# Kernel tuning notes

Measured on AMD Instinct MI355X. Metric: run time of the kernel, lower is better.

Reference implementation:

```python
import jax, jax.numpy as jnp
import numpy as np
from jax.scipy.linalg import solve_triangular

S = 64            # number of weight samples (Xi.shape[0])
OUT = 256         # out_channels
IN_CH, K = 64, 3
F = IN_CH * K * K # in_features == inducing_batch == 576
LOG_PREC_INIT = -4.0
LOG_PREC_LR = 1.0


def setup_inputs() -> dict:
    key = jax.random.key(0)
    k1, k2, k3, k4 = jax.random.split(key, 4)
    Xi = jax.random.normal(k1, (S, 128, F), jnp.float32)          # only shape[0] is used
    Xi_param = jax.random.normal(k2, (1, F, F), jnp.float32)      # self.Xi: [1, inducing_batch, in_features]
    u = jax.random.normal(k3, (OUT, F, 1), jnp.float32)           # self.u
    log_prec_scaled = (LOG_PREC_INIT / LOG_PREC_LR) * jnp.ones((1, 1, F), jnp.float32)
    Z = jax.random.normal(k4, (S, OUT, F, 1), jnp.float32)        # internal randn noise, made explicit
    return dict(Xi=Xi, Xi_param=Xi_param, u=u, log_prec_scaled=log_prec_scaled, Z=Z)


def reference(Xi, Xi_param, u, log_prec_scaled, Z):
    S_ = Xi.shape[0]
    Fd = Xi_param.shape[-1]
    O = u.shape[0]
    # log_prec = log_prec_lr * log_prec_scaled  (precs == 1)
    log_prec = LOG_PREC_LR * log_prec_scaled[0]                    # [1, F]
    Xe = jnp.broadcast_to(Xi_param, (S_, Fd, Fd))                  # [S, I, F]
    XiLT = jnp.exp(log_prec) * jnp.swapaxes(Xe, -1, -2)            # [S, F, I]  (prec_L is None branch)
    XiLXi = XiLT @ Xe                                              # [S, F, F]
    XiLY = jnp.einsum('sfi,oi->sfo', XiLT, u[..., 0])              # [S, F, O]  (torch: [S, O, F, 1])
    # NealPrior over in_shape: precision = fan_in * I, fan_in = in_features
    prior_prec = float(Fd)
    prec = XiLXi + prior_prec * jnp.eye(Fd, dtype=XiLXi.dtype)     # [S, F, F]
    L = jnp.linalg.cholesky(prec)
    logdet_prec = 2.0 * jnp.sum(jnp.log(jnp.diagonal(L, axis1=-2, axis2=-1)), -1)  # [S]
    logdet_prec_tot = O * logdet_prec                              # expand(S, O).sum(-1)
    # cholesky_solve(XiLY, L): prec^{-1} XiLY, batched over O via RHS columns
    mean = solve_triangular(L, solve_triangular(L, XiLY, lower=True), lower=True, trans=1)  # [S, F, O]
    Zm = jnp.swapaxes(Z[..., 0], -1, -2)                           # [S, F, O]
    dW = solve_triangular(L, Zm, lower=True, trans=1)              # L^T dW = Z
    sample_fo = mean + dW                                          # [S, F, O]
    sample = jnp.swapaxes(sample_fo, -1, -2)                       # [S, O, F] == self._sample
    # logP = mvnormal_log_prob_unnorm(prior_prec, sample^T):  -0.5 tr(x^T P x) + 0.5*O*logdet(P)
    logP = (-0.5 * prior_prec * jnp.sum(sample_fo ** 2, (-1, -2))
            + 0.5 * O * Fd * jnp.log(jnp.asarray(prior_prec, sample.dtype)))
    logQ = -0.5 * jnp.sum(Z ** 2, (-1, -2, -3)) + 0.5 * logdet_prec_tot
    logpq = logP - logQ                                            # [S]
    return sample, logpq
```

## Files before the change

### kernel.cpp

```cpp
#include <hip/hip_runtime.h>

#define F 576
#define OUTC 256
#define SNUM 64
#define PP 576.0f
#define NBLK 36

__device__ __forceinline__ void gbar(int* cnt, int barid) {
  __syncthreads();
  if (threadIdx.x == 0) {
    __builtin_amdgcn_fence(__ATOMIC_RELEASE, "agent");
    __hip_atomic_fetch_add(cnt, 1, __ATOMIC_RELAXED, __HIP_MEMORY_SCOPE_AGENT);
    int target = barid * NBLK;
    while (__hip_atomic_load(cnt, __ATOMIC_RELAXED, __HIP_MEMORY_SCOPE_AGENT) < target) {
      __builtin_amdgcn_s_sleep(2);
    }
    __builtin_amdgcn_fence(__ATOMIC_ACQUIRE, "agent");
  }
  __syncthreads();
}

__device__ __forceinline__ void mm16(const float (*As)[68], const float (*Bs)[68],
                                     float acc[4][4], int tx, int ty) {
#pragma unroll
  for (int k = 0; k < 32; ++k) {
    float4 a4 = *(const float4*)&As[k][ty * 4];
    float4 b4 = *(const float4*)&Bs[k][tx * 4];
    float av[4] = {a4.x, a4.y, a4.z, a4.w};
    float bv[4] = {b4.x, b4.y, b4.z, b4.w};
#pragma unroll
    for (int r = 0; r < 4; ++r)
#pragma unroll
      for (int c = 0; c < 4; ++c) acc[r][c] += av[r] * bv[c];
  }
}

__device__ void tile_gemm(const float* __restrict__ A, int lda,
                          const float* __restrict__ B, int ldb,
                          float* __restrict__ C, int ldc,
                          int m0, int n0, int K, float sgn,
                          float (*As)[68], float (*Bs)[68]) {
  int t = threadIdx.x, tx = t & 15, ty = t >> 4;
  float acc[4][4] = {};
  for (int k0 = 0; k0 < K; k0 += 32) {
    int rr = t >> 2, kq = t & 3;
    const float* ap = &A[(m0 + rr) * lda + k0 + kq * 8];
    float4 a0 = *(const float4*)ap;
    float4 a1 = *(const float4*)(ap + 4);
    As[kq*8+0][rr] = a0.x; As[kq*8+1][rr] = a0.y;
    As[kq*8+2][rr] = a0.z; As[kq*8+3][rr] = a0.w;
    As[kq*8+4][rr] = a1.x; As[kq*8+5][rr] = a1.y;
    As[kq*8+6][rr] = a1.z; As[kq*8+7][rr] = a1.w;
    int col = t & 63, kr = t >> 6;
#pragma unroll
    for (int kk = 0; kk < 32; kk += 4)
      Bs[kr + kk][col] = B[(k0 + kr + kk) * ldb + n0 + col];
    __syncthreads();
    mm16(As, Bs, acc, tx, ty);
    __syncthreads();
  }
#pragma unroll
  for (int r = 0; r < 4; ++r)
#pragma unroll
    for (int c = 0; c < 4; ++c)
      C[(m0 + ty*4 + r) * ldc + n0 + tx*4 + c] = sgn * acc[r][c];
}

__device__ void diag_factor(float* Ts ) {
  int t = threadIdx.x;
  __syncthreads();
  if (t < 64) {
    int l = t;
    float r[64];
#pragma unroll
    for (int g = 0; g < 64; ++g) r[g] = Ts[l*66 + g];
#pragma unroll
    for (int j = 0; j < 64; ++j) {
      float d = __shfl(r[j], j, 64);
      float inv = 1.0f / sqrtf(d);
      float c = r[j] * inv;
      r[j] = c;
#pragma unroll
      for (int g = j + 1; g < 64; ++g)
        r[g] = fmaf(-__shfl(c, g, 64), c, r[g]);
    }
#pragma unroll
    for (int g = 0; g < 64; ++g) Ts[l*66 + g] = r[g];
  }
  __syncthreads();
}

__device__ void panel_phase(float* __restrict__ G, int k0, int b,
                            float* Ts, float* invd) {
  int t = threadIdx.x;
  for (int idx = t; idx < 64 * 64; idx += 256) {
    int i = idx >> 6, j = idx & 63;
    Ts[i*66 + j] = G[(k0 + i) * F + k0 + j];
  }
  __syncthreads();
  if (t < 64) invd[t] = 1.0f / Ts[t*66 + t];
  __syncthreads();
  int l = t & 63, w = t >> 6;
  int r0 = k0 + 64 + b * 16 + w * 4;
  float v0 = G[(r0 + 0) * F + k0 + l];
  float v1 = G[(r0 + 1) * F + k0 + l];
  float v2 = G[(r0 + 2) * F + k0 + l];
  float v3 = G[(r0 + 3) * F + k0 + l];
#pragma unroll
  for (int j = 0; j < 64; ++j) {
    float dj = invd[j];
    float x0 = __shfl(v0, j, 64) * dj;
    float x1 = __shfl(v1, j, 64) * dj;
    float x2 = __shfl(v2, j, 64) * dj;
    float x3 = __shfl(v3, j, 64) * dj;
    if (l > j) {
      float lj = Ts[l*66 + j];
      v0 = fmaf(-x0, lj, v0);
      v1 = fmaf(-x1, lj, v1);
      v2 = fmaf(-x2, lj, v2);
      v3 = fmaf(-x3, lj, v3);
    }
  }
  float dl = invd[l];
  G[(r0 + 0) * F + k0 + l] = v0 * dl;
  G[(r0 + 1) * F + k0 + l] = v1 * dl;
  G[(r0 + 2) * F + k0 + l] = v2 * dl;
  G[(r0 + 3) * F + k0 + l] = v3 * dl;
}

__device__ void upd_phase(float* __restrict__ G, int k0, int ti, int tj, bool fuse,
                          float (*As)[68], float (*Bs)[68], float* Ts) {
  int b0 = k0 + 64;
  int i0 = b0 + ti * 64, j0 = b0 + tj * 64;
  int t = threadIdx.x, tx = t & 15, ty = t >> 4;
  float acc[4][4] = {};
  for (int kk0 = 0; kk0 < 64; kk0 += 32) {
    for (int idx = t; idx < 64 * 32; idx += 256) {
      int ii = idx >> 5, kk = idx & 31;
      As[kk][ii] = G[(i0 + ii) * F + k0 + kk0 + kk];
      Bs[kk][ii] = G[(j0 + ii) * F + k0 + kk0 + kk];
    }
    __syncthreads();
#pragma unroll
    for (int k = 0; k < 32; ++k) {
      float a[4], b[4];
#pragma unroll
      for (int m = 0; m < 4; ++m) { a[m] = As[k][ty*4 + m]; b[m] = Bs[k][tx*4 + m]; }
#pragma unroll
      for (int r = 0; r < 4; ++r)
#pragma unroll
        for (int c = 0; c < 4; ++c) acc[r][c] += a[r] * b[c];
    }
    __syncthreads();
  }
  if (!fuse) {
#pragma unroll
    for (int r = 0; r < 4; ++r)
#pragma unroll
      for (int c = 0; c < 4; ++c)
        G[(i0 + ty*4 + r) * F + j0 + tx*4 + c] -= acc[r][c];
  } else {
#pragma unroll
    for (int r = 0; r < 4; ++r)
#pragma unroll
      for (int c = 0; c < 4; ++c)
        Ts[(ty*4 + r)*66 + tx*4 + c] =
            G[(i0 + ty*4 + r) * F + j0 + tx*4 + c] - acc[r][c];
    diag_factor(Ts);
    for (int idx = t; idx < 64 * 64; idx += 256) {
      int i = idx >> 6, j = idx & 63;
      if (j <= i) G[(i0 + i) * F + j0 + j] = Ts[i*66 + j];
    }
  }
}

__device__ void base_inv_phase(const float* __restrict__ G, float* __restrict__ LI,
                               int blk, float* Ts, float* invd) {
  int base = blk * 64, t = threadIdx.x;
  for (int idx = t; idx < 64 * 64; idx += 256) {
    int i = idx >> 6, j = idx & 63;
    Ts[i*66 + j] = G[(base + i) * F + base + j];
  }
  __syncthreads();
  if (t < 64) invd[t] = 1.0f / Ts[t*66 + t];
  __syncthreads();
  int l = t & 63, w = t >> 6;
  float v[16];
#pragma unroll
  for (int c = 0; c < 16; ++c) v[c] = (l == (w * 16 + c)) ? 1.0f : 0.0f;
#pragma unroll
  for (int j = 0; j < 64; ++j) {
    float dj = invd[j];
    float lj = (l > j) ? Ts[l*66 + j] : 0.0f;
#pragma unroll
    for (int c = 0; c < 16; ++c) {
      float x = __shfl(v[c], j, 64) * dj;
      v[c] = fmaf(-x, lj, v[c]);
    }
  }
  float dl = invd[l];
#pragma unroll
  for (int c = 0; c < 16; ++c)
    LI[(base + l) * F + base + w * 16 + c] = v[c] * dl;
}

__device__ void mean_phase(const float* __restrict__ LI, const float* __restrict__ T,
                           float* __restrict__ meanT, int bf, int bo,
                           float (*As)[68], float (*Bs)[68]) {
  int t = threadIdx.x, tx = t & 15, ty = t >> 4;
  int f0 = bf * 64, o0 = bo * 64;
  float acc[4][4] = {};
  for (int g0 = f0; g0 < F; g0 += 32) {
    int col = t & 63, kr = t >> 6;
#pragma unroll
    for (int kk = 0; kk < 32; kk += 4) {
      As[kr + kk][col] = T[(g0 + kr + kk) * OUTC + o0 + col];
      Bs[kr + kk][col] = LI[(g0 + kr + kk) * F + f0 + col];
    }
    __syncthreads();
    mm16(As, Bs, acc, tx, ty);
    __syncthreads();
  }
#pragma unroll
  for (int r = 0; r < 4; ++r) {
    float4 st = make_float4(acc[r][0], acc[r][1], acc[r][2], acc[r][3]);
    *(float4*)&meanT[(o0 + ty*4 + r) * F + f0 + tx*4] = st;
  }
}

__global__ __launch_bounds__(256) void k_mid(float* __restrict__ G, float* __restrict__ LI,
                                             const float* __restrict__ Yb,
                                             float* __restrict__ Tb, float* __restrict__ meanT,
                                             int* __restrict__ ctl) {
  __shared__ float As[32][68];
  __shared__ float Bs[32][68];
  __shared__ float Ts[64 * 66];
  __shared__ float invd[64];
  int* cnt = ctl;
  int bar = 0;
  int b = blockIdx.x, t = threadIdx.x;
  float* Tw = Tb;

  if (b == 0) {
    for (int idx = t; idx < 64 * 64; idx += 256) {
      int i = idx >> 6, j = idx & 63;
      Ts[i*66 + j] = G[i * F + j];
    }
    diag_factor(Ts);
    for (int idx = t; idx < 64 * 64; idx += 256) {
      int i = idx >> 6, j = idx & 63;
      if (j <= i) G[i * F + j] = Ts[i*66 + j];
    }
  }
  gbar(cnt, ++bar);

  for (int k = 0; k < 8; ++k) {
    int k0 = k * 64;
    int n = 512 - k0;
    if (b < n / 16) panel_phase(G, k0, b, Ts, invd);
    gbar(cnt, ++bar);
    int nt = n / 64, ntiles = nt * (nt + 1) / 2;
    if (b < ntiles) {
      int ti = 0, bb = b;
      while (bb >= ti + 1) { bb -= ti + 1; ++ti; }
      int tj = bb;
      upd_phase(G, k0, ti, tj, (ti == 0 && tj == 0), As, Bs, Ts);
    }
    gbar(cnt, ++bar);
  }

  if (b < 9) {
    base_inv_phase(G, LI, b, Ts, invd);
  } else {
    int m = b - 9;
    for (int q = m; q < 72; q += 27) {
      int r = q / 8, cc = q % 8;
      int c = cc + (cc >= r ? 1 : 0);
      for (int idx = t; idx < 64 * 16; idx += 256) {
        int i = idx >> 4, jj = idx & 15;
        ((float4*)&LI[(r * 64 + i) * F + c * 64])[jj] = make_float4(0.f, 0.f, 0.f, 0.f);
      }
    }
  }
  gbar(cnt, ++bar);

  if (b < 4) tile_gemm(G + 64*F + b*128*(F+1), F, LI + b*128*(F+1), F,
                       Tw + b*4096, 64, 0, 0, 64, 1.0f, As, Bs);
  gbar(cnt, ++bar);
  if (b < 4) tile_gemm(LI + 64*(F+1) + b*128*(F+1), F, Tw + b*4096, 64,
                       LI + 64*F + b*128*(F+1), F, 0, 0, 64, -1.0f, As, Bs);
  gbar(cnt, ++bar);
  if (b < 8) {
    int z = b >> 2, tl = b & 3;
    tile_gemm(G + 128*F + z*256*(F+1), F, LI + z*256*(F+1), F,
              Tw + z*16384, 128, (tl>>1)*64, (tl&1)*64, 128, 1.0f, As, Bs);
  }
  gbar(cnt, ++bar);
  if (b < 8) {
    int z = b >> 2, tl = b & 3;
    tile_gemm(LI + 128*(F+1) + z*256*(F+1), F, Tw + z*16384, 128,
              LI + 128*F + z*256*(F+1), F, (tl>>1)*64, (tl&1)*64, 128, -1.0f, As, Bs);
  }
  gbar(cnt, ++bar);
  if (b < 16) tile_gemm(G + 256*F, F, LI, F, Tw, 256,
                        (b>>2)*64, (b&3)*64, 256, 1.0f, As, Bs);
  gbar(cnt, ++bar);
  if (b < 16) tile_gemm(LI + 256*(F+1), F, Tw, 256, LI + 256*F, F,
                        (b>>2)*64, (b&3)*64, 256, -1.0f, As, Bs);
  gbar(cnt, ++bar);
  if (b < 8) tile_gemm(G + 512*F, F, LI, F, Tw, 512, 0, b*64, 512, 1.0f, As, Bs);
  gbar(cnt, ++bar);
  if (b < 8) tile_gemm(LI + 512*(F+1), F, Tw, 512, LI + 512*F, F, 0, b*64, 64, -1.0f, As, Bs);
  gbar(cnt, ++bar);

  {
    int bg = b >> 2, bo = b & 3;
    tile_gemm(LI, F, Yb, OUTC, Tb, OUTC, bg * 64, bo * 64, bg * 64 + 64, 1.0f, As, Bs);
  }
  gbar(cnt, ++bar);

  {
    int bf = b >> 2, bo = b & 3;
    mean_phase(LI, Tb, meanT, bf, bo, As, Bs);
  }
}

__global__ __launch_bounds__(256) void k_gy(const float* __restrict__ X,
                                            const float* __restrict__ u,
                                            const float* __restrict__ lp,
                                            float* __restrict__ G,
                                            float* __restrict__ Y) {
  __shared__ float As[32][68];
  __shared__ float Bs[32][68];
  int t = threadIdx.x, tx = t & 15, ty = t >> 4;
  if (blockIdx.z == 0) {
    int bi = blockIdx.y, bj = blockIdx.x;
    if (bj > bi) return;
    int f0 = bi * 64, g0 = bj * 64;
    float acc[4][4] = {};
    for (int i0 = 0; i0 < F; i0 += 32) {
      int col = t & 63, kr = t >> 6;
#pragma unroll
      for (int kk = 0; kk < 32; kk += 4) {
        int i = i0 + kr + kk;
        float e = expf(lp[i]);
        As[kr + kk][col] = e * X[i * F + f0 + col];
        Bs[kr + kk][col] = X[i * F + g0 + col];
      }
      __syncthreads();
      mm16(As, Bs, acc, tx, ty);
      __syncthreads();
    }
#pragma unroll
    for (int r = 0; r < 4; ++r) {
      int gr = f0 + ty*4 + r;
#pragma unroll
      for (int c = 0; c < 4; ++c) {
        int gc = g0 + tx*4 + c;
        float v = acc[r][c];
        if (gr == gc) v += PP;
        G[gr * F + gc] = v;
      }
    }
  } else {
    if (blockIdx.x >= 4) return;
    int bo = blockIdx.x, bf = blockIdx.y;
    int f0 = bf * 64, o0 = bo * 64;
    float acc[4][4] = {};
    for (int i0 = 0; i0 < F; i0 += 32) {
      {
        int col = t & 63, kr = t >> 6;
#pragma unroll
        for (int kk = 0; kk < 32; kk += 4) {
          int i = i0 + kr + kk;
          As[kr + kk][col] = expf(lp[i]) * X[i * F + f0 + col];
        }
        int oo = t >> 2, kq = t & 3;
        const float* ur = &u[(o0 + oo) * F + i0 + kq * 8];
        float4 u0 = *(const float4*)ur;
        float4 u1 = *(const float4*)(ur + 4);
        Bs[kq*8+0][oo] = u0.x; Bs[kq*8+1][oo] = u0.y;
        Bs[kq*8+2][oo] = u0.z; Bs[kq*8+3][oo] = u0.w;
        Bs[kq*8+4][oo] = u1.x; Bs[kq*8+5][oo] = u1.y;
        Bs[kq*8+6][oo] = u1.z; Bs[kq*8+7][oo] = u1.w;
      }
      __syncthreads();
      mm16(As, Bs, acc, tx, ty);
      __syncthreads();
    }
#pragma unroll
    for (int r = 0; r < 4; ++r) {
      float4 st = make_float4(acc[r][0], acc[r][1], acc[r][2], acc[r][3]);
      *(float4*)&Y[(f0 + ty*4 + r) * OUTC + o0 + tx*4] = st;
    }
  }
}

__global__ __launch_bounds__(256) void k_big(const float* __restrict__ Z,
                                             const float* __restrict__ LI,
                                             const float* __restrict__ meanT,
                                             float* __restrict__ out,
                                             double* __restrict__ parts) {
  int bf = blockIdx.x, br = blockIdx.y;
  __shared__ float As[32][68];
  __shared__ float Bs[32][68];
  __shared__ double redA[256];
  __shared__ double redB[256];
  int t = threadIdx.x, tx = t & 15, ty = t >> 4;
  int f0 = bf * 64, r0 = br * 64;
  float acc[4][4] = {};
  double zsq = 0.0;
  for (int g0 = f0; g0 < F; g0 += 32) {
    {
      int rr = t >> 2, kq = t & 3;
      const float* zr = &Z[(r0 + rr) * F + g0 + kq * 8];
      float4 a0 = *(const float4*)zr;
      float4 a1 = *(const float4*)(zr + 4);
      if (bf == 0) {
        zsq += (double)a0.x*a0.x + (double)a0.y*a0.y + (double)a0.z*a0.z + (double)a0.w*a0.w
             + (double)a1.x*a1.x + (double)a1.y*a1.y + (double)a1.z*a1.z + (double)a1.w*a1.w;
      }
      As[kq*8+0][rr] = a0.x; As[kq*8+1][rr] = a0.y;
      As[kq*8+2][rr] = a0.z; As[kq*8+3][rr] = a0.w;
      As[kq*8+4][rr] = a1.x; As[kq*8+5][rr] = a1.y;
      As[kq*8+6][rr] = a1.z; As[kq*8+7][rr] = a1.w;
      int col = t & 63, kr = t >> 6;
#pragma unroll
      for (int kk = 0; kk < 32; kk += 4)
        Bs[kr + kk][col] = LI[(g0 + kr + kk) * F + f0 + col];
    }
    __syncthreads();
    mm16(As, Bs, acc, tx, ty);
    __syncthreads();
  }
  double ssq = 0.0;
#pragma unroll
  for (int r = 0; r < 4; ++r) {
    int row = r0 + ty*4 + r;
    int o = row & 255;
    float4 mv = *(const float4*)&meanT[o * F + f0 + tx*4];
    float4 st = make_float4(acc[r][0] + mv.x, acc[r][1] + mv.y,
                            acc[r][2] + mv.z, acc[r][3] + mv.w);
    *(float4*)&out[row * F + f0 + tx*4] = st;
    ssq += (double)st.x*st.x + (double)st.y*st.y + (double)st.z*st.z + (double)st.w*st.w;
  }
  redA[t] = ssq; redB[t] = zsq;
  __syncthreads();
  for (int o = 128; o > 0; o >>= 1) {
    if (t < o) { redA[t] += redA[t + o]; redB[t] += redB[t + o]; }
    __syncthreads();
  }
  if (t == 0) {
    int s = br >> 2;
    atomicAdd(&parts[s * 2 + 0], redA[0]);
    if (bf == 0) atomicAdd(&parts[s * 2 + 1], redB[0]);
  }
}

__global__ __launch_bounds__(576) void k_logpq_final(const float* __restrict__ LI,
                                                     const double* __restrict__ parts,
                                                     float* __restrict__ out) {
  __shared__ double red[576];
  int t = threadIdx.x;
  red[t] = log((double)LI[t * F + t]);
  __syncthreads();
  for (int o = 512; o > 0; o >>= 1) {
    if (t < o && t + o < 576) red[t] += red[t + o];
    __syncthreads();
  }
  double ldsumLI = red[0];
  if (t < SNUM) {
    double ssq = parts[t * 2 + 0];
    double zsq = parts[t * 2 + 1];
    double pp = 576.0;
    double lpq = -0.5 * pp * ssq
               + 0.5 * (double)(OUTC * F) * log(pp)
               + 0.5 * zsq
               + (double)OUTC * ldsumLI;
    out[SNUM * OUTC * F + t] = (float)lpq;
  }
}

extern "C" void kernel_launch(void* const* d_in, const int* in_sizes, int n_in,
                              void* d_out, int out_size, void* d_ws, size_t ws_size,
                              hipStream_t stream) {
  (void)in_sizes; (void)n_in; (void)out_size; (void)ws_size;
  const float* X  = (const float*)d_in[1];
  const float* u  = (const float*)d_in[2];
  const float* lp = (const float*)d_in[3];
  const float* Z  = (const float*)d_in[4];
  float* out = (float*)d_out;

  float* ws    = (float*)d_ws;
  float* G     = ws;
  float* LI    = ws + 331776;
  float* Yb    = ws + 663552;
  float* Tb    = ws + 811008;
  float* meanT = ws + 958464;
  double* parts = (double*)(ws + 1105920);
  int*    ctl   = (int*)(ws + 1105920 + 256);

  hipMemsetAsync((void*)(ws + 1105920), 0, 1032, stream);
  k_gy<<<dim3(9, 9, 2), 256, 0, stream>>>(X, u, lp, G, Yb);
  k_mid<<<NBLK, 256, 0, stream>>>(G, LI, Yb, Tb, meanT, ctl);
  k_big<<<dim3(9, 256), 256, 0, stream>>>(Z, LI, meanT, out, parts);
  k_logpq_final<<<1, 576, 0, stream>>>(LI, parts, out);
}
```

Before: 699.6 us.

## Use flag-based master grid barrier and merge dependent GEMM phases

```diff
diff --git a/kernel.cpp b/kernel.cpp
--- a/kernel.cpp
+++ b/kernel.cpp
@@ -5,15 +5,24 @@
 #define SNUM 64
 #define PP 576.0f
 #define NBLK 36
-
-__device__ __forceinline__ void gbar(int* cnt, int barid) {
+#define FLAG_STRIDE 32
+
+__device__ __forceinline__ void gbar(int* flags, int* gen, int b, int barid) {
   __syncthreads();
   if (threadIdx.x == 0) {
     __builtin_amdgcn_fence(__ATOMIC_RELEASE, "agent");
-    __hip_atomic_fetch_add(cnt, 1, __ATOMIC_RELAXED, __HIP_MEMORY_SCOPE_AGENT);
-    int target = barid * NBLK;
-    while (__hip_atomic_load(cnt, __ATOMIC_RELAXED, __HIP_MEMORY_SCOPE_AGENT) < target) {
-      __builtin_amdgcn_s_sleep(2);
+    __hip_atomic_store(&flags[b * FLAG_STRIDE], barid, __ATOMIC_RELAXED, __HIP_MEMORY_SCOPE_AGENT);
+    if (b == 0) {
+      for (int i = 1; i < NBLK; ++i) {
+        while (__hip_atomic_load(&flags[i * FLAG_STRIDE], __ATOMIC_RELAXED, __HIP_MEMORY_SCOPE_AGENT) < barid) {
+          __builtin_amdgcn_s_sleep(1);
+        }
+      }
+      __hip_atomic_store(gen, barid, __ATOMIC_RELAXED, __HIP_MEMORY_SCOPE_AGENT);
+    } else {
+      while (__hip_atomic_load(gen, __ATOMIC_RELAXED, __HIP_MEMORY_SCOPE_AGENT) < barid) {
+        __builtin_amdgcn_s_sleep(1);
+      }
     }
     __builtin_amdgcn_fence(__ATOMIC_ACQUIRE, "agent");
   }
@@ -231,12 +240,11 @@
 __global__ __launch_bounds__(256) void k_mid(float* __restrict__ G, float* __restrict__ LI,
                                              const float* __restrict__ Yb,
                                              float* __restrict__ Tb, float* __restrict__ meanT,
-                                             int* __restrict__ ctl) {
+                                             int* __restrict__ gen, int* __restrict__ flags) {
   __shared__ float As[32][68];
   __shared__ float Bs[32][68];
   __shared__ float Ts[64 * 66];
   __shared__ float invd[64];
-  int* cnt = ctl;
   int bar = 0;
   int b = blockIdx.x, t = threadIdx.x;
   float* Tw = Tb;
@@ -252,13 +260,13 @@
       if (j <= i) G[i * F + j] = Ts[i*66 + j];
     }
   }
-  gbar(cnt, ++bar);
+  gbar(flags, gen, b, ++bar);
 
   for (int k = 0; k < 8; ++k) {
     int k0 = k * 64;
     int n = 512 - k0;
     if (b < n / 16) panel_phase(G, k0, b, Ts, invd);
-    gbar(cnt, ++bar);
+    gbar(flags, gen, b, ++bar);
     int nt = n / 64, ntiles = nt * (nt + 1) / 2;
     if (b < ntiles) {
       int ti = 0, bb = b;
@@ -266,7 +274,7 @@
       int tj = bb;
       upd_phase(G, k0, ti, tj, (ti == 0 && tj == 0), As, Bs, Ts);
     }
-    gbar(cnt, ++bar);
+    gbar(flags, gen, b, ++bar);
   }
 
   if (b < 9) {
@@ -282,42 +290,44 @@
       }
     }
   }
-  gbar(cnt, ++bar);
-
-  if (b < 4) tile_gemm(G + 64*F + b*128*(F+1), F, LI + b*128*(F+1), F,
-                       Tw + b*4096, 64, 0, 0, 64, 1.0f, As, Bs);
-  gbar(cnt, ++bar);
-  if (b < 4) tile_gemm(LI + 64*(F+1) + b*128*(F+1), F, Tw + b*4096, 64,
-                       LI + 64*F + b*128*(F+1), F, 0, 0, 64, -1.0f, As, Bs);
-  gbar(cnt, ++bar);
+  gbar(flags, gen, b, ++bar);
+
+  if (b < 4) {
+    tile_gemm(G + 64*F + b*128*(F+1), F, LI + b*128*(F+1), F,
+              Tw + b*4096, 64, 0, 0, 64, 1.0f, As, Bs);
+    tile_gemm(LI + 64*(F+1) + b*128*(F+1), F, Tw + b*4096, 64,
+              LI + 64*F + b*128*(F+1), F, 0, 0, 64, -1.0f, As, Bs);
+  }
+  gbar(flags, gen, b, ++bar);
   if (b < 8) {
     int z = b >> 2, tl = b & 3;
     tile_gemm(G + 128*F + z*256*(F+1), F, LI + z*256*(F+1), F,
               Tw + z*16384, 128, (tl>>1)*64, (tl&1)*64, 128, 1.0f, As, Bs);
   }
-  gbar(cnt, ++bar);
+  gbar(flags, gen, b, ++bar);
   if (b < 8) {
     int z = b >> 2, tl = b & 3;
     tile_gemm(LI + 128*(F+1) + z*256*(F+1), F, Tw + z*16384, 128,
               LI + 128*F + z*256*(F+1), F, (tl>>1)*64, (tl&1)*64, 128, -1.0f, As, Bs);
   }
-  gbar(cnt, ++bar);
+  gbar(flags, gen, b, ++bar);
   if (b < 16) tile_gemm(G + 256*F, F, LI, F, Tw, 256,
                         (b>>2)*64, (b&3)*64, 256, 1.0f, As, Bs);
-  gbar(cnt, ++bar);
+  gbar(flags, gen, b, ++bar);
   if (b < 16) tile_gemm(LI + 256*(F+1), F, Tw, 256, LI + 256*F, F,
                         (b>>2)*64, (b&3)*64, 256, -1.0f, As, Bs);
-  gbar(cnt, ++bar);
-  if (b < 8) tile_gemm(G + 512*F, F, LI, F, Tw, 512, 0, b*64, 512, 1.0f, As, Bs);
-  gbar(cnt, ++bar);
-  if (b < 8) tile_gemm(LI + 512*(F+1), F, Tw, 512, LI + 512*F, F, 0, b*64, 64, -1.0f, As, Bs);
-  gbar(cnt, ++bar);
+  gbar(flags, gen, b, ++bar);
+  if (b < 8) {
+    tile_gemm(G + 512*F, F, LI, F, Tw, 512, 0, b*64, 512, 1.0f, As, Bs);
+    tile_gemm(LI + 512*(F+1), F, Tw, 512, LI + 512*F, F, 0, b*64, 64, -1.0f, As, Bs);
+  }
+  gbar(flags, gen, b, ++bar);
 
   {
     int bg = b >> 2, bo = b & 3;
     tile_gemm(LI, F, Yb, OUTC, Tb, OUTC, bg * 64, bo * 64, bg * 64 + 64, 1.0f, As, Bs);
   }
-  gbar(cnt, ++bar);
+  gbar(flags, gen, b, ++bar);
 
   {
     int bf = b >> 2, bo = b & 3;
@@ -498,11 +508,12 @@
   float* Tb    = ws + 811008;
   float* meanT = ws + 958464;
   double* parts = (double*)(ws + 1105920);
-  int*    ctl   = (int*)(ws + 1105920 + 256);
-
-  hipMemsetAsync((void*)(ws + 1105920), 0, 1032, stream);
+  int*    gen   = (int*)(ws + 1105920 + 256);
+  int*    flags = (int*)(ws + 1105920 + 288);
+
+  hipMemsetAsync((void*)(ws + 1105920), 0, 8192, stream);
   k_gy<<<dim3(9, 9, 2), 256, 0, stream>>>(X, u, lp, G, Yb);
-  k_mid<<<NBLK, 256, 0, stream>>>(G, LI, Yb, Tb, meanT, ctl);
+  k_mid<<<NBLK, 256, 0, stream>>>(G, LI, Yb, Tb, meanT, gen, flags);
   k_big<<<dim3(9, 256), 256, 0, stream>>>(Z, LI, meanT, out, parts);
   k_logpq_final<<<1, 576, 0, stream>>>(LI, parts, out);
 }
```

Measured after the change: 942.2 us. +34.7%, slower.

## Replace recursive blocked L-inverse with column-strip forward/backward substitution solves

Applied to the files above, without the earlier changes.

```diff
diff --git a/kernel.cpp b/kernel.cpp
--- a/kernel.cpp
+++ b/kernel.cpp
@@ -35,35 +35,148 @@
   }
 }
 
-__device__ void tile_gemm(const float* __restrict__ A, int lda,
-                          const float* __restrict__ B, int ldb,
-                          float* __restrict__ C, int ldc,
-                          int m0, int n0, int K, float sgn,
-                          float (*As)[68], float (*Bs)[68]) {
+__device__ __forceinline__ void mmqs(const float (*As)[68], const float (*Xs)[20],
+                                     float acc[4], int tx, int ty) {
+#pragma unroll
+  for (int k = 0; k < 32; ++k) {
+    float4 a4 = *(const float4*)&As[k][ty * 4];
+    float b = Xs[k][tx];
+    acc[0] += a4.x * b; acc[1] += a4.y * b;
+    acc[2] += a4.z * b; acc[3] += a4.w * b;
+  }
+}
+
+__device__ __forceinline__ void stageA_T(const float* __restrict__ M, int lda, int h,
+                                         float (*As)[68]) {
+  int t = threadIdx.x, rr = t >> 2, kq = t & 3;
+  const float* ap = &M[rr * lda + h * 32 + kq * 8];
+  float4 a0 = *(const float4*)ap;
+  float4 a1 = *(const float4*)(ap + 4);
+  As[kq*8+0][rr] = a0.x; As[kq*8+1][rr] = a0.y;
+  As[kq*8+2][rr] = a0.z; As[kq*8+3][rr] = a0.w;
+  As[kq*8+4][rr] = a1.x; As[kq*8+5][rr] = a1.y;
+  As[kq*8+6][rr] = a1.z; As[kq*8+7][rr] = a1.w;
+}
+
+__device__ __forceinline__ void stageA_N(const float* __restrict__ M, int lda, int h,
+                                         float (*As)[68]) {
+  int t = threadIdx.x, col = t & 63, kr = t >> 6;
+#pragma unroll
+  for (int kk = 0; kk < 32; kk += 4)
+    As[kr + kk][col] = M[(h * 32 + kr + kk) * lda + col];
+}
+
+__device__ __forceinline__ void stageX(const float* __restrict__ src, int ldx, int c0, int h,
+                                       float (*Xs)[20]) {
+  int t = threadIdx.x, k = t >> 3, c = (t & 7) * 2;
+  Xs[k][c]     = src[(h * 32 + k) * ldx + c0 + c];
+  Xs[k][c + 1] = src[(h * 32 + k) * ldx + c0 + c + 1];
+}
+
+__device__ __forceinline__ void stageX_T(const float* __restrict__ src, int ldsrc, int c0,
+                                         int poff, int h, float (*Xs)[20]) {
+  int t = threadIdx.x, k = t >> 3, c = (t & 7) * 2;
+  Xs[k][c]     = src[(c0 + c) * ldsrc + poff + h * 32 + k];
+  Xs[k][c + 1] = src[(c0 + c + 1) * ldsrc + poff + h * 32 + k];
+}
+
+__device__ void solve_LI(const float* __restrict__ G, float* __restrict__ LI,
+                         int j, int q, float (*As)[68], float (*Xs)[20]) {
   int t = threadIdx.x, tx = t & 15, ty = t >> 4;
-  float acc[4][4] = {};
-  for (int k0 = 0; k0 < K; k0 += 32) {
-    int rr = t >> 2, kq = t & 3;
-    const float* ap = &A[(m0 + rr) * lda + k0 + kq * 8];
-    float4 a0 = *(const float4*)ap;
-    float4 a1 = *(const float4*)(ap + 4);
-    As[kq*8+0][rr] = a0.x; As[kq*8+1][rr] = a0.y;
-    As[kq*8+2][rr] = a0.z; As[kq*8+3][rr] = a0.w;
-    As[kq*8+4][rr] = a1.x; As[kq*8+5][rr] = a1.y;
-    As[kq*8+6][rr] = a1.z; As[kq*8+7][rr] = a1.w;
-    int col = t & 63, kr = t >> 6;
-#pragma unroll
-    for (int kk = 0; kk < 32; kk += 4)
-      Bs[kr + kk][col] = B[(k0 + kr + kk) * ldb + n0 + col];
-    __syncthreads();
-    mm16(As, Bs, acc, tx, ty);
-    __syncthreads();
-  }
-#pragma unroll
-  for (int r = 0; r < 4; ++r)
-#pragma unroll
-    for (int c = 0; c < 4; ++c)
-      C[(m0 + ty*4 + r) * ldc + n0 + tx*4 + c] = sgn * acc[r][c];
+  int c0 = j * 64 + q * 16;
+  for (int i = j + 1; i <= 8; ++i) {
+    float acc[4] = {0.f, 0.f, 0.f, 0.f};
+    for (int p = j; p < i; ++p)
+      for (int h = 0; h < 2; ++h) {
+        __syncthreads();
+        stageA_T(&G[(i * 64) * F + p * 64], F, h, As);
+        stageX(&LI[(p * 64) * F], F, c0, h, Xs);
+        __syncthreads();
+        mmqs(As, Xs, acc, tx, ty);
+      }
+    float out[4] = {0.f, 0.f, 0.f, 0.f};
+    for (int h = 0; h < 2; ++h) {
+      __syncthreads();
+      if ((ty >> 3) == h) {
+        int rl = (ty & 7) * 4;
+        Xs[rl+0][tx] = -acc[0]; Xs[rl+1][tx] = -acc[1];
+        Xs[rl+2][tx] = -acc[2]; Xs[rl+3][tx] = -acc[3];
+      }
+      stageA_T(&LI[(i * 64) * F + i * 64], F, h, As);
+      __syncthreads();
+      mmqs(As, Xs, out, tx, ty);
+    }
+#pragma unroll
+    for (int m = 0; m < 4; ++m)
+      LI[(i * 64 + ty * 4 + m) * F + c0 + tx] = out[m];
+  }
+}
+
+__device__ void solve_T(const float* __restrict__ G, const float* __restrict__ LI,
+                        const float* __restrict__ Yb, float* __restrict__ Tb,
+                        int q16, float (*As)[68], float (*Xs)[20]) {
+  int t = threadIdx.x, tx = t & 15, ty = t >> 4;
+  int c0 = q16 * 16;
+  for (int i = 0; i <= 8; ++i) {
+    float acc[4] = {0.f, 0.f, 0.f, 0.f};
+    for (int p = 0; p < i; ++p)
+      for (int h = 0; h < 2; ++h) {
+        __syncthreads();
+        stageA_T(&G[(i * 64) * F + p * 64], F, h, As);
+        stageX(&Tb[(p * 64) * OUTC], OUTC, c0, h, Xs);
+        __syncthreads();
+        mmqs(As, Xs, acc, tx, ty);
+      }
+    float out[4] = {0.f, 0.f, 0.f, 0.f};
+    for (int h = 0; h < 2; ++h) {
+      __syncthreads();
+      if ((ty >> 3) == h) {
+        int rl = (ty & 7) * 4;
+#pragma unroll
+        for (int m = 0; m < 4; ++m)
+          Xs[rl + m][tx] = Yb[(i * 64 + h * 32 + rl + m) * OUTC + c0 + tx] - acc[m];
+      }
+      stageA_T(&LI[(i * 64) * F + i * 64], F, h, As);
+      __syncthreads();
+      mmqs(As, Xs, out, tx, ty);
+    }
+#pragma unroll
+    for (int m = 0; m < 4; ++m)
+      Tb[(i * 64 + ty * 4 + m) * OUTC + c0 + tx] = out[m];
+  }
+}
+
+__device__ void solve_M(const float* __restrict__ G, const float* __restrict__ LI,
+                        const float* __restrict__ Tb, float* __restrict__ meanT,
+                        int q16, float (*As)[68], float (*Xs)[20]) {
+  int t = threadIdx.x, tx = t & 15, ty = t >> 4;
+  int c0 = q16 * 16;
+  for (int i = 8; i >= 0; --i) {
+    float acc[4] = {0.f, 0.f, 0.f, 0.f};
+    for (int p = i + 1; p <= 8; ++p)
+      for (int h = 0; h < 2; ++h) {
+        __syncthreads();
+        stageA_N(&G[(p * 64) * F + i * 64], F, h, As);
+        stageX_T(meanT, F, c0, p * 64, h, Xs);
+        __syncthreads();
+        mmqs(As, Xs, acc, tx, ty);
+      }
+    float out[4] = {0.f, 0.f, 0.f, 0.f};
+    for (int h = 0; h < 2; ++h) {
+      __syncthreads();
+      if ((ty >> 3) == h) {
+        int rl = (ty & 7) * 4;
+#pragma unroll
+        for (int m = 0; m < 4; ++m)
+          Xs[rl + m][tx] = Tb[(i * 64 + h * 32 + rl + m) * OUTC + c0 + tx] - acc[m];
+      }
+      stageA_N(&LI[(i * 64) * F + i * 64], F, h, As);
+      __syncthreads();
+      mmqs(As, Xs, out, tx, ty);
+    }
+    float4 st = make_float4(out[0], out[1], out[2], out[3]);
+    *(float4*)&meanT[(c0 + tx) * F + i * 64 + ty * 4] = st;
+  }
 }
 
 __device__ void diag_factor(float* Ts ) {
@@ -204,42 +317,17 @@
     LI[(base + l) * F + base + w * 16 + c] = v[c] * dl;
 }
 
-__device__ void mean_phase(const float* __restrict__ LI, const float* __restrict__ T,
-                           float* __restrict__ meanT, int bf, int bo,
-                           float (*As)[68], float (*Bs)[68]) {
-  int t = threadIdx.x, tx = t & 15, ty = t >> 4;
-  int f0 = bf * 64, o0 = bo * 64;
-  float acc[4][4] = {};
-  for (int g0 = f0; g0 < F; g0 += 32) {
-    int col = t & 63, kr = t >> 6;
-#pragma unroll
-    for (int kk = 0; kk < 32; kk += 4) {
-      As[kr + kk][col] = T[(g0 + kr + kk) * OUTC + o0 + col];
-      Bs[kr + kk][col] = LI[(g0 + kr + kk) * F + f0 + col];
-    }
-    __syncthreads();
-    mm16(As, Bs, acc, tx, ty);
-    __syncthreads();
-  }
-#pragma unroll
-  for (int r = 0; r < 4; ++r) {
-    float4 st = make_float4(acc[r][0], acc[r][1], acc[r][2], acc[r][3]);
-    *(float4*)&meanT[(o0 + ty*4 + r) * F + f0 + tx*4] = st;
-  }
-}
-
 __global__ __launch_bounds__(256) void k_mid(float* __restrict__ G, float* __restrict__ LI,
                                              const float* __restrict__ Yb,
                                              float* __restrict__ Tb, float* __restrict__ meanT,
-                                             int* __restrict__ ctl) {
+                                             int* __restrict__ cnt) {
   __shared__ float As[32][68];
   __shared__ float Bs[32][68];
   __shared__ float Ts[64 * 66];
   __shared__ float invd[64];
-  int* cnt = ctl;
+  __shared__ float Xs[32][20];
   int bar = 0;
   int b = blockIdx.x, t = threadIdx.x;
-  float* Tw = Tb;
 
   if (b == 0) {
     for (int idx = t; idx < 64 * 64; idx += 256) {
@@ -272,10 +360,11 @@
   if (b < 9) {
     base_inv_phase(G, LI, b, Ts, invd);
   } else {
-    int m = b - 9;
-    for (int q = m; q < 72; q += 27) {
-      int r = q / 8, cc = q % 8;
-      int c = cc + (cc >= r ? 1 : 0);
+    int m0 = b - 9;
+    for (int mm = m0; mm < 36; mm += 27) {
+      int r = 0, rem = mm;
+      while (rem >= 8 - r) { rem -= 8 - r; ++r; }
+      int c = r + 1 + rem;
       for (int idx = t; idx < 64 * 16; idx += 256) {
         int i = idx >> 4, jj = idx & 15;
         ((float4*)&LI[(r * 64 + i) * F + c * 64])[jj] = make_float4(0.f, 0.f, 0.f, 0.f);
@@ -284,45 +373,11 @@
   }
   gbar(cnt, ++bar);
 
-  if (b < 4) tile_gemm(G + 64*F + b*128*(F+1), F, LI + b*128*(F+1), F,
-                       Tw + b*4096, 64, 0, 0, 64, 1.0f, As, Bs);
+  if (b < 32) solve_LI(G, LI, b >> 2, b & 3, As, Xs);
+  if (b >= 20) solve_T(G, LI, Yb, Tb, b - 20, As, Xs);
   gbar(cnt, ++bar);
-  if (b < 4) tile_gemm(LI + 64*(F+1) + b*128*(F+1), F, Tw + b*4096, 64,
-                       LI + 64*F + b*128*(F+1), F, 0, 0, 64, -1.0f, As, Bs);
-  gbar(cnt, ++bar);
-  if (b < 8) {
-    int z = b >> 2, tl = b & 3;
-    tile_gemm(G + 128*F + z*256*(F+1), F, LI + z*256*(F+1), F,
-              Tw + z*16384, 128, (tl>>1)*64, (tl&1)*64, 128, 1.0f, As, Bs);
-  }
-  gbar(cnt, ++bar);
-  if (b < 8) {
-    int z = b >> 2, tl = b & 3;
-    tile_gemm(LI + 128*(F+1) + z*256*(F+1), F, Tw + z*16384, 128,
-              LI + 128*F + z*256*(F+1), F, (tl>>1)*64, (tl&1)*64, 128, -1.0f, As, Bs);
-  }
-  gbar(cnt, ++bar);
-  if (b < 16) tile_gemm(G + 256*F, F, LI, F, Tw, 256,
-                        (b>>2)*64, (b&3)*64, 256, 1.0f, As, Bs);
-  gbar(cnt, ++bar);
-  if (b < 16) tile_gemm(LI + 256*(F+1), F, Tw, 256, LI + 256*F, F,
-                        (b>>2)*64, (b&3)*64, 256, -1.0f, As, Bs);
-  gbar(cnt, ++bar);
-  if (b < 8) tile_gemm(G + 512*F, F, LI, F, Tw, 512, 0, b*64, 512, 1.0f, As, Bs);
-  gbar(cnt, ++bar);
-  if (b < 8) tile_gemm(LI + 512*(F+1), F, Tw, 512, LI + 512*F, F, 0, b*64, 64, -1.0f, As, Bs);
-  gbar(cnt, ++bar);
-
-  {
-    int bg = b >> 2, bo = b & 3;
-    tile_gemm(LI, F, Yb, OUTC, Tb, OUTC, bg * 64, bo * 64, bg * 64 + 64, 1.0f, As, Bs);
-  }
-  gbar(cnt, ++bar);
-
-  {
-    int bf = b >> 2, bo = b & 3;
-    mean_phase(LI, Tb, meanT, bf, bo, As, Bs);
-  }
+
+  if (b < 16) solve_M(G, LI, Tb, meanT, b, As, Xs);
 }
 
 __global__ __launch_bounds__(256) void k_gy(const float* __restrict__ X,
@@ -498,11 +553,11 @@
   float* Tb    = ws + 811008;
   float* meanT = ws + 958464;
   double* parts = (double*)(ws + 1105920);
-  int*    ctl   = (int*)(ws + 1105920 + 256);
+  int*    cnt   = (int*)(ws + 1105920 + 256);
 
   hipMemsetAsync((void*)(ws + 1105920), 0, 1032, stream);
   k_gy<<<dim3(9, 9, 2), 256, 0, stream>>>(X, u, lp, G, Yb);
-  k_mid<<<NBLK, 256, 0, stream>>>(G, LI, Yb, Tb, meanT, ctl);
+  k_mid<<<NBLK, 256, 0, stream>>>(G, LI, Yb, Tb, meanT, cnt);
   k_big<<<dim3(9, 256), 256, 0, stream>>>(Z, LI, meanT, out, parts);
   k_logpq_final<<<1, 576, 0, stream>>>(LI, parts, out);
 }
```

Result: slower. 797.9 us (+14.0%).

## Fuse panel TRSM into trailing update to halve Cholesky grid barriers

Applied to the files above, without the earlier changes.

```diff
diff --git a/kernel.cpp b/kernel.cpp
--- a/kernel.cpp
+++ b/kernel.cpp
@@ -66,6 +66,31 @@
       C[(m0 + ty*4 + r) * ldc + n0 + tx*4 + c] = sgn * acc[r][c];
 }
 
+__device__ void tile_gemm_up(const float* __restrict__ Aup,
+                             const float* __restrict__ B, int ldb,
+                             float* __restrict__ C, int ldc,
+                             int m0, int n0, int K, float sgn,
+                             float (*As)[68], float (*Bs)[68]) {
+  int t = threadIdx.x, tx = t & 15, ty = t >> 4;
+  float acc[4][4] = {};
+  for (int k0 = 0; k0 < K; k0 += 32) {
+    int col = t & 63, kr = t >> 6;
+#pragma unroll
+    for (int kk = 0; kk < 32; kk += 4) {
+      As[kr + kk][col] = Aup[(k0 + kr + kk) * F + m0 + col];
+      Bs[kr + kk][col] = B[(k0 + kr + kk) * ldb + n0 + col];
+    }
+    __syncthreads();
+    mm16(As, Bs, acc, tx, ty);
+    __syncthreads();
+  }
+#pragma unroll
+  for (int r = 0; r < 4; ++r)
+#pragma unroll
+    for (int c = 0; c < 4; ++c)
+      C[(m0 + ty*4 + r) * ldc + n0 + tx*4 + c] = sgn * acc[r][c];
+}
+
 __device__ void diag_factor(float* Ts ) {
   int t = threadIdx.x;
   __syncthreads();
@@ -90,9 +115,45 @@
   __syncthreads();
 }
 
-__device__ void panel_phase(float* __restrict__ G, int k0, int b,
-                            float* Ts, float* invd) {
-  int t = threadIdx.x;
+__device__ void trsm64(const float* __restrict__ G, int rowbase, int k0,
+                       const float* Ts, const float* invd, float* PT) {
+  int t = threadIdx.x, l = t & 63, w = t >> 6;
+  for (int pass = 0; pass < 4; ++pass) {
+    int lr = pass * 16 + w * 4;
+    int r0 = rowbase + lr;
+    float v0 = G[(r0 + 0) * F + k0 + l];
+    float v1 = G[(r0 + 1) * F + k0 + l];
+    float v2 = G[(r0 + 2) * F + k0 + l];
+    float v3 = G[(r0 + 3) * F + k0 + l];
+#pragma unroll
+    for (int j = 0; j < 64; ++j) {
+      float dj = invd[j];
+      float x0 = __shfl(v0, j, 64) * dj;
+      float x1 = __shfl(v1, j, 64) * dj;
+      float x2 = __shfl(v2, j, 64) * dj;
+      float x3 = __shfl(v3, j, 64) * dj;
+      if (l > j) {
+        float lj = Ts[l*66 + j];
+        v0 = fmaf(-x0, lj, v0);
+        v1 = fmaf(-x1, lj, v1);
+        v2 = fmaf(-x2, lj, v2);
+        v3 = fmaf(-x3, lj, v3);
+      }
+    }
+    float dl = invd[l];
+    PT[l*68 + lr + 0] = v0 * dl;
+    PT[l*68 + lr + 1] = v1 * dl;
+    PT[l*68 + lr + 2] = v2 * dl;
+    PT[l*68 + lr + 3] = v3 * dl;
+  }
+}
+
+__device__ void chol_phase(float* __restrict__ G, int k, int ti, int tj,
+                           float* Ts, float* invd, float* PaT, float* PbT) {
+  int k0 = k * 64;
+  int bi = k0 + 64 + ti * 64;
+  int bj = k0 + 64 + tj * 64;
+  int t = threadIdx.x, tx = t & 15, ty = t >> 4;
   for (int idx = t; idx < 64 * 64; idx += 256) {
     int i = idx >> 6, j = idx & 63;
     Ts[i*66 + j] = G[(k0 + i) * F + k0 + j];
@@ -100,77 +161,47 @@
   __syncthreads();
   if (t < 64) invd[t] = 1.0f / Ts[t*66 + t];
   __syncthreads();
-  int l = t & 63, w = t >> 6;
-  int r0 = k0 + 64 + b * 16 + w * 4;
-  float v0 = G[(r0 + 0) * F + k0 + l];
-  float v1 = G[(r0 + 1) * F + k0 + l];
-  float v2 = G[(r0 + 2) * F + k0 + l];
-  float v3 = G[(r0 + 3) * F + k0 + l];
-#pragma unroll
-  for (int j = 0; j < 64; ++j) {
-    float dj = invd[j];
-    float x0 = __shfl(v0, j, 64) * dj;
-    float x1 = __shfl(v1, j, 64) * dj;
-    float x2 = __shfl(v2, j, 64) * dj;
-    float x3 = __shfl(v3, j, 64) * dj;
-    if (l > j) {
-      float lj = Ts[l*66 + j];
-      v0 = fmaf(-x0, lj, v0);
-      v1 = fmaf(-x1, lj, v1);
-      v2 = fmaf(-x2, lj, v2);
-      v3 = fmaf(-x3, lj, v3);
-    }
-  }
-  float dl = invd[l];
-  G[(r0 + 0) * F + k0 + l] = v0 * dl;
-  G[(r0 + 1) * F + k0 + l] = v1 * dl;
-  G[(r0 + 2) * F + k0 + l] = v2 * dl;
-  G[(r0 + 3) * F + k0 + l] = v3 * dl;
-}
-
-__device__ void upd_phase(float* __restrict__ G, int k0, int ti, int tj, bool fuse,
-                          float (*As)[68], float (*Bs)[68], float* Ts) {
-  int b0 = k0 + 64;
-  int i0 = b0 + ti * 64, j0 = b0 + tj * 64;
-  int t = threadIdx.x, tx = t & 15, ty = t >> 4;
+  trsm64(G, bi, k0, Ts, invd, PaT);
+  if (tj < ti) trsm64(G, bj, k0, Ts, invd, PbT);
+  __syncthreads();
+  const float* PjT = (tj < ti) ? PbT : PaT;
   float acc[4][4] = {};
-  for (int kk0 = 0; kk0 < 64; kk0 += 32) {
-    for (int idx = t; idx < 64 * 32; idx += 256) {
-      int ii = idx >> 5, kk = idx & 31;
-      As[kk][ii] = G[(i0 + ii) * F + k0 + kk0 + kk];
-      Bs[kk][ii] = G[(j0 + ii) * F + k0 + kk0 + kk];
-    }
-    __syncthreads();
-#pragma unroll
-    for (int k = 0; k < 32; ++k) {
-      float a[4], b[4];
-#pragma unroll
-      for (int m = 0; m < 4; ++m) { a[m] = As[k][ty*4 + m]; b[m] = Bs[k][tx*4 + m]; }
-#pragma unroll
-      for (int r = 0; r < 4; ++r)
-#pragma unroll
-        for (int c = 0; c < 4; ++c) acc[r][c] += a[r] * b[c];
-    }
-    __syncthreads();
-  }
-  if (!fuse) {
+#pragma unroll 4
+  for (int kk = 0; kk < 64; ++kk) {
+    float4 a4 = *(const float4*)&PaT[kk*68 + ty * 4];
+    float4 b4 = *(const float4*)&PjT[kk*68 + tx * 4];
+    float av[4] = {a4.x, a4.y, a4.z, a4.w};
+    float bv[4] = {b4.x, b4.y, b4.z, b4.w};
 #pragma unroll
     for (int r = 0; r < 4; ++r)
 #pragma unroll
-      for (int c = 0; c < 4; ++c)
-        G[(i0 + ty*4 + r) * F + j0 + tx*4 + c] -= acc[r][c];
-  } else {
+      for (int c = 0; c < 4; ++c) acc[r][c] += av[r] * bv[c];
+  }
+  if (tj == 0) {
+    for (int idx = t; idx < 64 * 64; idx += 256) {
+      int c = idx >> 6, r = idx & 63;
+      G[(k0 + c) * F + bi + r] = PaT[c*68 + r];
+    }
+  }
+  if (ti == 0 && tj == 0) {
+    __syncthreads();
 #pragma unroll
     for (int r = 0; r < 4; ++r)
 #pragma unroll
       for (int c = 0; c < 4; ++c)
         Ts[(ty*4 + r)*66 + tx*4 + c] =
-            G[(i0 + ty*4 + r) * F + j0 + tx*4 + c] - acc[r][c];
+            G[(bi + ty*4 + r) * F + bj + tx*4 + c] - acc[r][c];
     diag_factor(Ts);
     for (int idx = t; idx < 64 * 64; idx += 256) {
       int i = idx >> 6, j = idx & 63;
-      if (j <= i) G[(i0 + i) * F + j0 + j] = Ts[i*66 + j];
-    }
+      if (j <= i) G[(bi + i) * F + bj + j] = Ts[i*66 + j];
+    }
+  } else {
+#pragma unroll
+    for (int r = 0; r < 4; ++r)
+#pragma unroll
+      for (int c = 0; c < 4; ++c)
+        G[(bi + ty*4 + r) * F + bj + tx*4 + c] -= acc[r][c];
   }
 }
 
@@ -231,12 +262,13 @@
 __global__ __launch_bounds__(256) void k_mid(float* __restrict__ G, float* __restrict__ LI,
                                              const float* __restrict__ Yb,
                                              float* __restrict__ Tb, float* __restrict__ meanT,
-                                             int* __restrict__ ctl) {
+                                             int* __restrict__ cnt) {
   __shared__ float As[32][68];
   __shared__ float Bs[32][68];
   __shared__ float Ts[64 * 66];
   __shared__ float invd[64];
-  int* cnt = ctl;
+  __shared__ float PaT[64 * 68];
+  __shared__ float PbT[64 * 68];
   int bar = 0;
   int b = blockIdx.x, t = threadIdx.x;
   float* Tw = Tb;
@@ -255,16 +287,11 @@
   gbar(cnt, ++bar);
 
   for (int k = 0; k < 8; ++k) {
-    int k0 = k * 64;
-    int n = 512 - k0;
-    if (b < n / 16) panel_phase(G, k0, b, Ts, invd);
-    gbar(cnt, ++bar);
-    int nt = n / 64, ntiles = nt * (nt + 1) / 2;
+    int nt = 8 - k, ntiles = nt * (nt + 1) / 2;
     if (b < ntiles) {
       int ti = 0, bb = b;
       while (bb >= ti + 1) { bb -= ti + 1; ++ti; }
-      int tj = bb;
-      upd_phase(G, k0, ti, tj, (ti == 0 && tj == 0), As, Bs, Ts);
+      chol_phase(G, k, ti, bb, Ts, invd, PaT, PbT);
     }
     gbar(cnt, ++bar);
   }
@@ -284,16 +311,17 @@
   }
   gbar(cnt, ++bar);
 
-  if (b < 4) tile_gemm(G + 64*F + b*128*(F+1), F, LI + b*128*(F+1), F,
-                       Tw + b*4096, 64, 0, 0, 64, 1.0f, As, Bs);
-  gbar(cnt, ++bar);
-  if (b < 4) tile_gemm(LI + 64*(F+1) + b*128*(F+1), F, Tw + b*4096, 64,
-                       LI + 64*F + b*128*(F+1), F, 0, 0, 64, -1.0f, As, Bs);
+  if (b < 4) {
+    tile_gemm_up(G + b*128*(F+1) + 64, LI + b*128*(F+1), F,
+                 Tw + b*4096, 64, 0, 0, 64, 1.0f, As, Bs);
+    tile_gemm(LI + 64*(F+1) + b*128*(F+1), F, Tw + b*4096, 64,
+              LI + 64*F + b*128*(F+1), F, 0, 0, 64, -1.0f, As, Bs);
+  }
   gbar(cnt, ++bar);
   if (b < 8) {
     int z = b >> 2, tl = b & 3;
-    tile_gemm(G + 128*F + z*256*(F+1), F, LI + z*256*(F+1), F,
-              Tw + z*16384, 128, (tl>>1)*64, (tl&1)*64, 128, 1.0f, As, Bs);
+    tile_gemm_up(G + z*256*(F+1) + 128, LI + z*256*(F+1), F,
+                 Tw + z*16384, 128, (tl>>1)*64, (tl&1)*64, 128, 1.0f, As, Bs);
   }
   gbar(cnt, ++bar);
   if (b < 8) {
@@ -302,15 +330,16 @@
               LI + 128*F + z*256*(F+1), F, (tl>>1)*64, (tl&1)*64, 128, -1.0f, As, Bs);
   }
   gbar(cnt, ++bar);
-  if (b < 16) tile_gemm(G + 256*F, F, LI, F, Tw, 256,
-                        (b>>2)*64, (b&3)*64, 256, 1.0f, As, Bs);
+  if (b < 16) tile_gemm_up(G + 256, LI, F, Tw, 256,
+                           (b>>2)*64, (b&3)*64, 256, 1.0f, As, Bs);
   gbar(cnt, ++bar);
   if (b < 16) tile_gemm(LI + 256*(F+1), F, Tw, 256, LI + 256*F, F,
                         (b>>2)*64, (b&3)*64, 256, -1.0f, As, Bs);
   gbar(cnt, ++bar);
-  if (b < 8) tile_gemm(G + 512*F, F, LI, F, Tw, 512, 0, b*64, 512, 1.0f, As, Bs);
-  gbar(cnt, ++bar);
-  if (b < 8) tile_gemm(LI + 512*(F+1), F, Tw, 512, LI + 512*F, F, 0, b*64, 64, -1.0f, As, Bs);
+  if (b < 8) {
+    tile_gemm_up(G + 512, LI, F, Tw, 512, 0, b*64, 512, 1.0f, As, Bs);
+    tile_gemm(LI + 512*(F+1), F, Tw, 512, LI + 512*F, F, 0, b*64, 64, -1.0f, As, Bs);
+  }
   gbar(cnt, ++bar);
 
   {
@@ -498,11 +527,11 @@
   float* Tb    = ws + 811008;
   float* meanT = ws + 958464;
   double* parts = (double*)(ws + 1105920);
-  int*    ctl   = (int*)(ws + 1105920 + 256);
+  int*    cnt   = (int*)(ws + 1105920 + 256);
 
   hipMemsetAsync((void*)(ws + 1105920), 0, 1032, stream);
   k_gy<<<dim3(9, 9, 2), 256, 0, stream>>>(X, u, lp, G, Yb);
-  k_mid<<<NBLK, 256, 0, stream>>>(G, LI, Yb, Tb, meanT, ctl);
+  k_mid<<<NBLK, 256, 0, stream>>>(G, LI, Yb, Tb, meanT, cnt);
   k_big<<<dim3(9, 256), 256, 0, stream>>>(Z, LI, meanT, out, parts);
   k_logpq_final<<<1, 576, 0, stream>>>(LI, parts, out);
 }
```

New measurement: 774.1 us. +10.6%, slower.
